# Performance work log

Measured on AMD Instinct MI355X. Metric: run time of the kernel, lower is better.

The kernel has to match this reference:

```python
import jax, jax.numpy as jnp
import numpy as np

S = 32            # state: nodes per graph, conv output channels
B = 4096          # number of graphs
N = B * S         # total nodes
E = 2 * 1024 * 1024  # total edges (avg degree 16)
A = 2             # action_space_dimension
NACT = 32         # number_of_actions (adv heads)
EPS = 1e-5


def setup_inputs() -> dict:
    key = jax.random.key(0)
    ks = jax.random.split(key, 24)
    f = lambda k, sh, s: (jax.random.normal(k, sh, jnp.float32) * s)
    return {
        'x': f(ks[0], (N, 2), 1.0),
        'edge_index': jax.random.randint(ks[1], (2, E), 0, N),
        # conv1 MLP: Linear(4,16) -> ReLU -> Linear(16,S)
        'c1W1': f(ks[2], (4, 16), 0.5), 'c1b1': jnp.zeros((16,), jnp.float32),
        'c1W2': f(ks[3], (16, S), 0.25), 'c1b2': jnp.zeros((S,), jnp.float32),
        # conv2/conv3 MLPs: Linear(2*S,16) -> ReLU -> Linear(16,S)
        'c2W1': f(ks[4], (2 * S, 16), 0.12), 'c2b1': jnp.zeros((16,), jnp.float32),
        'c2W2': f(ks[5], (16, S), 0.25), 'c2b2': jnp.zeros((S,), jnp.float32),
        'c3W1': f(ks[6], (2 * S, 16), 0.12), 'c3b1': jnp.zeros((16,), jnp.float32),
        'c3W2': f(ks[7], (16, S), 0.25), 'c3b2': jnp.zeros((S,), jnp.float32),
        # 3 BatchNorm1d(S) layers (stacked)
        'bn_g': jnp.ones((3, S), jnp.float32), 'bn_b': jnp.zeros((3, S), jnp.float32),
        # dense head MLP 1024->256->256->256
        'mW1': f(ks[8], (S * S, 256), 0.03), 'mb1': jnp.zeros((256,), jnp.float32),
        'mW2': f(ks[9], (256, 256), 0.06), 'mb2': jnp.zeros((256,), jnp.float32),
        'mW3': f(ks[10], (256, 256), 0.06), 'mb3': jnp.zeros((256,), jnp.float32),
        # dueling heads
        'vW': f(ks[11], (256, 1), 0.06), 'vb': jnp.zeros((1,), jnp.float32),
        'aW': f(ks[12], (NACT, 256, A), 0.06), 'ab': jnp.zeros((NACT, A), jnp.float32),
    }


def _edgeconv(x, src, dst, W1, b1, W2, b2):
    # PyG EdgeConv with aggr='add': msg = MLP(cat[x_i, x_j - x_i]), summed at target i
    xi = x[dst]                       # [E, F]
    xj = x[src]                       # [E, F]
    m = jnp.concatenate([xi, xj - xi], axis=-1)        # [E, 2F]
    h = jnp.maximum(m @ W1 + b1, 0.0) @ W2 + b2        # [E, S]
    return jax.ops.segment_sum(h, dst, num_segments=x.shape[0])  # [N, S]


def _bn(h, g, b):
    # BatchNorm1d in training mode: batch stats over node dim, biased variance
    mu = h.mean(axis=0)
    var = jnp.mean((h - mu) ** 2, axis=0)
    return (h - mu) * jax.lax.rsqrt(var + EPS) * g + b


def reference(x, edge_index, c1W1, c1b1, c1W2, c1b2, c2W1, c2b1, c2W2, c2b2,
              c3W1, c3b1, c3W2, c3b2, bn_g, bn_b, mW1, mb1, mW2, mb2,
              mW3, mb3, vW, vb, aW, ab):
    src, dst = edge_index[0], edge_index[1]
    h = _edgeconv(x, src, dst, c1W1, c1b1, c1W2, c1b2)
    h = jax.nn.relu(_bn(h, bn_g[0], bn_b[0]))
    h = _edgeconv(h, src, dst, c2W1, c2b1, c2W2, c2b2)
    h = jax.nn.relu(_bn(h, bn_g[1], bn_b[1]))
    h = _edgeconv(h, src, dst, c3W1, c3b1, c3W2, c3b2)
    h = jax.nn.relu(_bn(h, bn_g[2], bn_b[2]))
    nb = x.shape[0] // S                                 # graphs in batch
    out = h.reshape(nb, S * S)                           # [B, in_size]
    out = jax.nn.relu(out @ mW1 + mb1)
    out = jax.nn.relu(out @ mW2 + mb2)
    out = jax.nn.relu(out @ mW3 + mb3)                   # [B, 256]
    value = out @ vW + vb                                # [B, 1]
    adv = jnp.einsum('bf,nfa->bna', out, aW) + ab        # [B, NACT, A]
    q = value[:, :, None] + adv - adv.mean(axis=2, keepdims=True)
    return q
```

## Files before the change

### kernel.cpp

```cpp
#include <hip/hip_runtime.h>
#include <hip/hip_fp16.h>

#define NN 131072
#define EE 2097152
#define SS 32
#define HH 16
#define BB 4096
#define EPS 1e-5f

#define BKT 512
#define BNODES 256
#define CAP 4864
#define SCAP 8192
#define TILE 8192

typedef _Float16 f16x8 __attribute__((ext_vector_type(8)));
typedef _Float16 f16x4 __attribute__((ext_vector_type(4)));
typedef float f32x4 __attribute__((ext_vector_type(4)));

__global__ __launch_bounds__(1024) void k_bsort(const int* __restrict__ ei, int* __restrict__ gcount,
                                                int* __restrict__ words) {
    __shared__ int cnt[BKT];
    __shared__ int tstart[BKT];
    __shared__ int gshift[BKT];
    __shared__ int sc[BKT];
    __shared__ int sword[TILE];
    __shared__ int sdst[TILE];
    int t = threadIdx.x;
    if (t < BKT) cnt[t] = 0;
    __syncthreads();
    int e0 = blockIdx.x * TILE;
    int dreg[TILE / 1024];
#pragma unroll
    for (int it = 0; it < TILE / 1024; ++it) {
        dreg[it] = ei[EE + e0 + it * 1024 + t];
        atomicAdd(&cnt[dreg[it] >> 8], 1);
    }
    __syncthreads();
    int val = (t < BKT) ? cnt[t] : 0;
    if (t < BKT) sc[t] = val;
    __syncthreads();
    for (int d = 1; d < BKT; d <<= 1) {
        int v2 = (t >= d && t < BKT) ? sc[t - d] : 0;
        __syncthreads();
        if (t < BKT) sc[t] += v2;
        __syncthreads();
    }
    if (t < BKT) {
        int excl = sc[t] - val;
        tstart[t] = excl;
        gshift[t] = t * CAP + atomicAdd(&gcount[t], val) - excl;
        cnt[t] = 0;
    }
    __syncthreads();
#pragma unroll
    for (int it = 0; it < TILE / 1024; ++it) {
        int e = e0 + it * 1024 + t;
        int src = ei[e];
        int dst = dreg[it];
        int b = dst >> 8;
        int r = atomicAdd(&cnt[b], 1);
        int p = tstart[b] + r;
        sword[p] = src | ((dst & 255) << 17);
        sdst[p] = gshift[b] + p;
    }
    __syncthreads();
#pragma unroll
    for (int it = 0; it < TILE / 1024; ++it) {
        int i = it * 1024 + t;
        words[sdst[i]] = sword[i];
    }
}

__global__ __launch_bounds__(512) void k_csr(const int* __restrict__ words, const int* __restrict__ gcount,
                                             int* __restrict__ ssrc, int* __restrict__ offs,
                                             int* __restrict__ offe) {
    __shared__ int hist[BNODES];
    __shared__ int sc[BNODES];
    __shared__ int base[BNODES];
    int t = threadIdx.x;
    int b = blockIdx.x;
    if (t < BNODES) hist[t] = 0;
    __syncthreads();
    int cnt = gcount[b];
    const int* wp = words + (size_t)b * CAP;
    int wreg[10];
#pragma unroll
    for (int it = 0; it < 10; ++it) {
        int p = t + it * 512;
        int w = (p < cnt) ? wp[p] : -1;
        wreg[it] = w;
        if (w >= 0) atomicAdd(&hist[w >> 17], 1);
    }
    __syncthreads();
    int val = 0, pval = 0;
    if (t < BNODES) {
        val = hist[t];
        pval = (val + 15) & ~15;
        sc[t] = pval;
    }
    __syncthreads();
    for (int d = 1; d < BNODES; d <<= 1) {
        int v2 = (t >= d && t < BNODES) ? sc[t - d] : 0;
        __syncthreads();
        if (t < BNODES) sc[t] += v2;
        __syncthreads();
    }
    int gbase = b * SCAP;
    if (t < BNODES) {
        base[t] = sc[t] - pval;
        offs[b * BNODES + t] = gbase + base[t];
        offe[b * BNODES + t] = gbase + base[t] + val;
        hist[t] = 0;
    }
    __syncthreads();
#pragma unroll
    for (int it = 0; it < 10; ++it) {
        int w = wreg[it];
        if (w >= 0) {
            int dl = w >> 17;
            int r = atomicAdd(&hist[dl], 1);
            ssrc[gbase + base[dl] + r] = w & 0x1FFFF;
        }
    }
    if (t < BNODES) {
        int s = gbase + base[t];
        for (int i = val; i < pval; ++i) ssrc[s + i] = NN;
    }
}

__global__ __launch_bounds__(256) void k_prep(const float* __restrict__ mW1, const float* __restrict__ mW2,
                                              const float* __restrict__ mW3, const float* __restrict__ vW,
                                              const float* __restrict__ vb, const float* __restrict__ aW,
                                              const float* __restrict__ ab,
                                              _Float16* __restrict__ W1T, _Float16* __restrict__ W2T,
                                              _Float16* __restrict__ W3T, _Float16* __restrict__ BqT,
                                              float* __restrict__ biasq, int* __restrict__ gcount,
                                              float* __restrict__ bns,
                                              const float* __restrict__ x, const float* __restrict__ c1W1,
                                              const float* __restrict__ c1b1,
                                              float* __restrict__ u, __half* __restrict__ v) {
    int i = blockIdx.x * 256 + threadIdx.x;
    {
        int n = i >> 4, c = i & 15;
        float x0 = x[n * 2], x1 = x[n * 2 + 1];
        float w0 = c1W1[c], w1 = c1W1[16 + c], w2 = c1W1[32 + c], w3 = c1W1[48 + c];
        u[i] = c1b1[c] + x0 * (w0 - w2) + x1 * (w1 - w3);
        v[i] = __float2half(x0 * w2 + x1 * w3);
    }
    if (i < 262144) {
        int k = i >> 8, n = i & 255;
        W1T[(size_t)n * 1024 + k] = (_Float16)mW1[i];
    }
    if (i < 65536) {
        int k = i >> 8, n = i & 255;
        W2T[n * 256 + k] = (_Float16)mW2[i];
        W3T[n * 256 + k] = (_Float16)mW3[i];
    }
    if (i < 16384) {
        int f = i >> 6, j = i & 63;
        int n = j >> 1, a = j & 1;
        float wa = aW[n * 512 + f * 2 + a];
        float wo = aW[n * 512 + f * 2 + (1 - a)];
        BqT[j * 256 + f] = (_Float16)(vW[f] + 0.5f * (wa - wo));
    }
    if (i < 64) biasq[i] = vb[0] + 0.5f * (ab[i] - ab[i ^ 1]);
    if (i < 512) gcount[i] = 0;
    if (i < 1536) bns[i] = 0.f;
    if (i < 16) v[NN * 16 + i] = __float2half(-60000.0f);
}

__global__ __launch_bounds__(256) void k_bnpre(const float* __restrict__ y, const float* __restrict__ bns,
                                               const float* __restrict__ g, const float* __restrict__ bb,
                                               const float* __restrict__ W1, const float* __restrict__ b1,
                                               float* __restrict__ u, __half* __restrict__ v) {
    __shared__ float sh[16][33];
    __shared__ float wd[32][16];
    __shared__ float wv[32][16];
    __shared__ float scL[32], soL[32];
    int t = threadIdx.x;
    if (t < 32) {
        float sm = 0.f, sq = 0.f;
#pragma unroll
        for (int s = 0; s < 8; ++s) { sm += bns[s * 64 + t]; sq += bns[s * 64 + 32 + t]; }
        const float inv_n = 1.0f / (float)NN;
        float mean = sm * inv_n;
        float var = sq * inv_n - mean * mean;
        float s2 = g[t] * rsqrtf(var + EPS);
        scL[t] = s2;
        soL[t] = bb[t] - mean * s2;
    }
    for (int i = t; i < 512; i += 256) {
        int f = i >> 4, c = i & 15;
        float wt = W1[i];
        float wb = W1[512 + i];
        wd[f][c] = wt - wb;
        wv[f][c] = wb;
    }
    __syncthreads();
    int nb = blockIdx.x * 16;
    for (int i = t; i < 512; i += 256) {
        int col = i & 31;
        sh[i >> 5][col] = fmaxf(y[nb * 32 + i] * scL[col] + soL[col], 0.f);
    }
    __syncthreads();
    int c = t & 15, nl = t >> 4;
    float uu = b1[c], vv = 0.f;
#pragma unroll
    for (int f = 0; f < 32; ++f) {
        float hv = sh[nl][f];
        uu += hv * wd[f][c];
        vv += hv * wv[f][c];
    }
    int n = nb + nl;
    u[n * 16 + c] = uu;
    v[n * 16 + c] = __float2half(vv);
    if (blockIdx.x == 0 && t < 16) v[NN * 16 + t] = __float2half(-60000.0f);
}

__global__ __launch_bounds__(256) void k_gather(const float* __restrict__ u, const __half* __restrict__ v,
                                                const int* __restrict__ ssrc, const int* __restrict__ offs,
                                                const int* __restrict__ offe,
                                                const float* __restrict__ W2, const float* __restrict__ b2,
                                                float* __restrict__ y, float* __restrict__ bns) {
    __shared__ float sw2[512];
    __shared__ float sagg[32 * 18];
    __shared__ float cntL[32];
    __shared__ float ssum[32];
    __shared__ float ssq[32];
    int t = threadIdx.x;
    if (t < 32) { ssum[t] = 0.f; ssq[t] = 0.f; }
    float w2a = W2[t], w2b = W2[t + 256];
    float b2r0 = b2[(t & 7) * 4], b2r1 = b2[(t & 7) * 4 + 1];
    float b2r2 = b2[(t & 7) * 4 + 2], b2r3 = b2[(t & 7) * 4 + 3];
    int nl = t >> 3, c2 = t & 7;
    int n = blockIdx.x * 32 + nl;
    int s0 = offs[n], e0 = offe[n];
    int pe = s0 + ((e0 - s0 + 15) & ~15);
    float2 uc = *(const float2*)(u + (size_t)n * 16 + 2 * c2);
    float a0 = 0.f, a1 = 0.f;
    for (int p = s0; p < pe; p += 16) {
        int idx[16];
#pragma unroll
        for (int i = 0; i < 16; ++i) idx[i] = ssrc[p + i];
        float2 vv[16];
#pragma unroll
        for (int i = 0; i < 16; ++i)
            vv[i] = __half22float2(*(const __half2*)(v + (size_t)idx[i] * 16 + 2 * c2));
#pragma unroll
        for (int i = 0; i < 16; ++i) {
            a0 += fmaxf(uc.x + vv[i].x, 0.f);
            a1 += fmaxf(uc.y + vv[i].y, 0.f);
        }
    }
    sagg[nl * 18 + 2 * c2] = a0;
    sagg[nl * 18 + 2 * c2 + 1] = a1;
    if (c2 == 0) cntL[nl] = (float)(e0 - s0);
    sw2[t] = w2a;
    sw2[t + 256] = w2b;
    __syncthreads();
    int node = t >> 3, oc = (t & 7) * 4;
    float cw = cntL[node];
    float o0 = b2r0 * cw, o1 = b2r1 * cw, o2 = b2r2 * cw, o3 = b2r3 * cw;
#pragma unroll
    for (int k = 0; k < 16; ++k) {
        float a = sagg[node * 18 + k];
        o0 += a * sw2[k * 32 + oc];
        o1 += a * sw2[k * 32 + oc + 1];
        o2 += a * sw2[k * 32 + oc + 2];
        o3 += a * sw2[k * 32 + oc + 3];
    }
    *(float4*)(y + (size_t)(blockIdx.x * 32 + node) * 32 + oc) = make_float4(o0, o1, o2, o3);
    float q0 = o0 * o0, q1 = o1 * o1, q2 = o2 * o2, q3 = o3 * o3;
#pragma unroll
    for (int m = 8; m < 64; m <<= 1) {
        o0 += __shfl_xor(o0, m); o1 += __shfl_xor(o1, m);
        o2 += __shfl_xor(o2, m); o3 += __shfl_xor(o3, m);
        q0 += __shfl_xor(q0, m); q1 += __shfl_xor(q1, m);
        q2 += __shfl_xor(q2, m); q3 += __shfl_xor(q3, m);
    }
    if ((t & 63) < 8) {
        atomicAdd(&ssum[oc], o0);     atomicAdd(&ssum[oc + 1], o1);
        atomicAdd(&ssum[oc + 2], o2); atomicAdd(&ssum[oc + 3], o3);
        atomicAdd(&ssq[oc], q0);      atomicAdd(&ssq[oc + 1], q1);
        atomicAdd(&ssq[oc + 2], q2);  atomicAdd(&ssq[oc + 3], q3);
    }
    __syncthreads();
    if (t < 64) {
        float val = (t < 32) ? ssum[t] : ssq[t - 32];
        atomicAdd(&bns[(blockIdx.x & 7) * 64 + t], val);
    }
}

__global__ __launch_bounds__(256) void k_bnrelu16(const float* __restrict__ y, const float* __restrict__ bns,
                                                  const float* __restrict__ g, const float* __restrict__ bb,
                                                  _Float16* __restrict__ h16) {
    __shared__ float sc_[32], sh_[32];
    int t = threadIdx.x;
    if (t < 32) {
        float sm = 0.f, sq = 0.f;
#pragma unroll
        for (int s = 0; s < 8; ++s) { sm += bns[s * 64 + t]; sq += bns[s * 64 + 32 + t]; }
        const float inv_n = 1.0f / (float)NN;
        float mean = sm * inv_n;
        float var = sq * inv_n - mean * mean;
        float sc = g[t] * rsqrtf(var + EPS);
        sc_[t] = sc;
        sh_[t] = bb[t] - mean * sc;
    }
    __syncthreads();
    int i = (blockIdx.x * 256 + t) * 4;
    float4 v4 = *(const float4*)(y + i);
    int j = i & 31;
    f16x4 o;
    o[0] = (_Float16)fmaxf(v4.x * sc_[j] + sh_[j], 0.f);
    o[1] = (_Float16)fmaxf(v4.y * sc_[j + 1] + sh_[j + 1], 0.f);
    o[2] = (_Float16)fmaxf(v4.z * sc_[j + 2] + sh_[j + 2], 0.f);
    o[3] = (_Float16)fmaxf(v4.w * sc_[j + 3] + sh_[j + 3], 0.f);
    *(f16x4*)(h16 + i) = o;
}

__global__ __launch_bounds__(256) void k_mgemm(const _Float16* __restrict__ A, const _Float16* __restrict__ BT,
                                               const float* __restrict__ bias, float* __restrict__ Cf,
                                               _Float16* __restrict__ Ch, int M, int N, int K,
                                               int relu, int out16) {
    int tid = threadIdx.x;
    int w = tid >> 6, l = tid & 63, q = l >> 4, r = l & 15;
    int rowBase = blockIdx.x * 64;
    int col = blockIdx.y * 64 + w * 16 + r;
    const _Float16* ap = A + (size_t)(rowBase + r) * K + q * 8;
    const _Float16* bp = BT + (size_t)col * K + q * 8;
    f32x4 z = {0.f, 0.f, 0.f, 0.f};
    f32x4 acc[4] = {z, z, z, z};
    for (int k0 = 0; k0 < K; k0 += 32) {
        f16x8 bf = *(const f16x8*)(bp + k0);
        f16x8 a0 = *(const f16x8*)(ap + k0);
        f16x8 a1 = *(const f16x8*)(ap + k0 + (size_t)16 * K);
        f16x8 a2 = *(const f16x8*)(ap + k0 + (size_t)32 * K);
        f16x8 a3 = *(const f16x8*)(ap + k0 + (size_t)48 * K);
        acc[0] = __builtin_amdgcn_mfma_f32_16x16x32_f16(a0, bf, acc[0], 0, 0, 0);
        acc[1] = __builtin_amdgcn_mfma_f32_16x16x32_f16(a1, bf, acc[1], 0, 0, 0);
        acc[2] = __builtin_amdgcn_mfma_f32_16x16x32_f16(a2, bf, acc[2], 0, 0, 0);
        acc[3] = __builtin_amdgcn_mfma_f32_16x16x32_f16(a3, bf, acc[3], 0, 0, 0);
    }
    float bv = bias[col];
#pragma unroll
    for (int rt = 0; rt < 4; ++rt) {
#pragma unroll
        for (int i = 0; i < 4; ++i) {
            int row = rowBase + rt * 16 + q * 4 + i;
            float val = acc[rt][i] + bv;
            if (relu) val = fmaxf(val, 0.f);
            if (out16) Ch[(size_t)row * N + col] = (_Float16)val;
            else       Cf[(size_t)row * N + col] = val;
        }
    }
}

extern "C" void kernel_launch(void* const* d_in, const int* in_sizes, int n_in,
                              void* d_out, int out_size, void* d_ws, size_t ws_size,
                              hipStream_t stream) {
    const float* x    = (const float*)d_in[0];
    const int*   ei   = (const int*)d_in[1];
    const float* c1W1 = (const float*)d_in[2];
    const float* c1b1 = (const float*)d_in[3];
    const float* c1W2 = (const float*)d_in[4];
    const float* c1b2 = (const float*)d_in[5];
    const float* c2W1 = (const float*)d_in[6];
    const float* c2b1 = (const float*)d_in[7];
    const float* c2W2 = (const float*)d_in[8];
    const float* c2b2 = (const float*)d_in[9];
    const float* c3W1 = (const float*)d_in[10];
    const float* c3b1 = (const float*)d_in[11];
    const float* c3W2 = (const float*)d_in[12];
    const float* c3b2 = (const float*)d_in[13];
    const float* bn_g = (const float*)d_in[14];
    const float* bn_b = (const float*)d_in[15];
    const float* mW1  = (const float*)d_in[16];
    const float* mb1  = (const float*)d_in[17];
    const float* mW2  = (const float*)d_in[18];
    const float* mb2  = (const float*)d_in[19];
    const float* mW3  = (const float*)d_in[20];
    const float* mb3  = (const float*)d_in[21];
    const float* vW   = (const float*)d_in[22];
    const float* vb   = (const float*)d_in[23];
    const float* aW   = (const float*)d_in[24];
    const float* ab   = (const float*)d_in[25];
    float* out = (float*)d_out;

    char* p = (char*)d_ws;
    auto take = [&](size_t bytes) {
        char* r = p;
        p += (bytes + 255) & ~(size_t)255;
        return r;
    };
    int*       gcount = (int*)take((size_t)BKT * 4);
    int*       words  = (int*)take((size_t)BKT * CAP * 4);
    int*       ssrc   = (int*)take((size_t)BKT * SCAP * 4);
    int*       offs   = (int*)take((size_t)NN * 4);
    int*       offe   = (int*)take((size_t)NN * 4);
    float*     u      = (float*)take((size_t)NN * HH * 4);
    __half*    v      = (__half*)take((size_t)(NN + 1) * HH * 2);
    float*     y      = (float*)take((size_t)NN * SS * 4);
    _Float16*  h16    = (_Float16*)take((size_t)NN * SS * 2);
    float*     bns    = (float*)take(3 * 512 * 4);
    _Float16*  W1T    = (_Float16*)take((size_t)256 * 1024 * 2);
    _Float16*  W2T    = (_Float16*)take((size_t)256 * 256 * 2);
    _Float16*  W3T    = (_Float16*)take((size_t)256 * 256 * 2);
    _Float16*  BqT    = (_Float16*)take((size_t)64 * 256 * 2);
    float*     biasq  = (float*)take(64 * 4);
    _Float16*  Xa     = (_Float16*)take((size_t)BB * 256 * 2);
    _Float16*  Xb     = (_Float16*)take((size_t)BB * 256 * 2);

    k_prep<<<NN * 16 / 256, 256, 0, stream>>>(mW1, mW2, mW3, vW, vb, aW, ab,
                                              W1T, W2T, W3T, BqT, biasq, gcount, bns,
                                              x, c1W1, c1b1, u, v);

    k_bsort<<<EE / TILE, 1024, 0, stream>>>(ei, gcount, words);
    k_csr<<<BKT, 512, 0, stream>>>(words, gcount, ssrc, offs, offe);

    k_gather<<<NN / 32, 256, 0, stream>>>(u, v, ssrc, offs, offe, c1W2, c1b2, y, bns);
    k_bnpre<<<NN / 16, 256, 0, stream>>>(y, bns, bn_g, bn_b, c2W1, c2b1, u, v);
    k_gather<<<NN / 32, 256, 0, stream>>>(u, v, ssrc, offs, offe, c2W2, c2b2, y, bns + 512);
    k_bnpre<<<NN / 16, 256, 0, stream>>>(y, bns + 512, bn_g + 32, bn_b + 32, c3W1, c3b1, u, v);
    k_gather<<<NN / 32, 256, 0, stream>>>(u, v, ssrc, offs, offe, c3W2, c3b2, y, bns + 1024);
    k_bnrelu16<<<NN * 32 / 1024, 256, 0, stream>>>(y, bns + 1024, bn_g + 64, bn_b + 64, h16);

    k_mgemm<<<dim3(BB / 64, 4), 256, 0, stream>>>(h16, W1T, mb1, nullptr, Xa, BB, 256, 1024, 1, 1);
    k_mgemm<<<dim3(BB / 64, 4), 256, 0, stream>>>(Xa, W2T, mb2, nullptr, Xb, BB, 256, 256, 1, 1);
    k_mgemm<<<dim3(BB / 64, 4), 256, 0, stream>>>(Xb, W3T, mb3, nullptr, Xa, BB, 256, 256, 1, 1);
    k_mgemm<<<dim3(BB / 64, 1), 256, 0, stream>>>(Xa, BqT, biasq, out, nullptr, BB, 64, 256, 0, 0);
}
```

Baseline: 307.0 us.

## Fuse dense MLP head into one kernel and widen gather loads per thread

The four separate MFMA GEMM launches for the dense head become one kernel in which each block keeps a 32-row tile of activations in shared memory across all layers, so the intermediate activation buffers never go to global memory and three launches are dropped. The gather kernel now gives each thread four channels of a node, 64 nodes per block, and loads 8-byte fp16 vectors instead of 4-byte ones, which halves the number of scattered loads per edge. In exchange the fused MLP launches only 128 blocks, which limits parallelism, and each block re-reads the full weight matrices.

```diff
diff --git a/kernel.cpp b/kernel.cpp
--- a/kernel.cpp
+++ b/kernel.cpp
@@ -224,8 +224,8 @@
                                                 const float* __restrict__ W2, const float* __restrict__ b2,
                                                 float* __restrict__ y, float* __restrict__ bns) {
     __shared__ float sw2[512];
-    __shared__ float sagg[32 * 18];
-    __shared__ float cntL[32];
+    __shared__ float sagg[64 * 17];
+    __shared__ float cntL[64];
     __shared__ float ssum[32];
     __shared__ float ssq[32];
     int t = threadIdx.x;
@@ -233,57 +233,66 @@
     float w2a = W2[t], w2b = W2[t + 256];
     float b2r0 = b2[(t & 7) * 4], b2r1 = b2[(t & 7) * 4 + 1];
     float b2r2 = b2[(t & 7) * 4 + 2], b2r3 = b2[(t & 7) * 4 + 3];
-    int nl = t >> 3, c2 = t & 7;
-    int n = blockIdx.x * 32 + nl;
+    int nl = t >> 2, c4 = t & 3;
+    int n = blockIdx.x * 64 + nl;
     int s0 = offs[n], e0 = offe[n];
     int pe = s0 + ((e0 - s0 + 15) & ~15);
-    float2 uc = *(const float2*)(u + (size_t)n * 16 + 2 * c2);
-    float a0 = 0.f, a1 = 0.f;
+    float4 uc = *(const float4*)(u + (size_t)n * 16 + 4 * c4);
+    float a0 = 0.f, a1 = 0.f, a2 = 0.f, a3 = 0.f;
     for (int p = s0; p < pe; p += 16) {
         int idx[16];
 #pragma unroll
         for (int i = 0; i < 16; ++i) idx[i] = ssrc[p + i];
-        float2 vv[16];
+        uint2 hv[16];
 #pragma unroll
         for (int i = 0; i < 16; ++i)
-            vv[i] = __half22float2(*(const __half2*)(v + (size_t)idx[i] * 16 + 2 * c2));
+            hv[i] = *(const uint2*)(v + (size_t)idx[i] * 16 + 4 * c4);
 #pragma unroll
         for (int i = 0; i < 16; ++i) {
-            a0 += fmaxf(uc.x + vv[i].x, 0.f);
-            a1 += fmaxf(uc.y + vv[i].y, 0.f);
-        }
-    }
-    sagg[nl * 18 + 2 * c2] = a0;
-    sagg[nl * 18 + 2 * c2 + 1] = a1;
-    if (c2 == 0) cntL[nl] = (float)(e0 - s0);
+            float2 f01 = __half22float2(*(const __half2*)&hv[i].x);
+            float2 f23 = __half22float2(*(const __half2*)&hv[i].y);
+            a0 += fmaxf(uc.x + f01.x, 0.f);
+            a1 += fmaxf(uc.y + f01.y, 0.f);
+            a2 += fmaxf(uc.z + f23.x, 0.f);
+            a3 += fmaxf(uc.w + f23.y, 0.f);
+        }
+    }
+    sagg[nl * 17 + 4 * c4]     = a0;
+    sagg[nl * 17 + 4 * c4 + 1] = a1;
+    sagg[nl * 17 + 4 * c4 + 2] = a2;
+    sagg[nl * 17 + 4 * c4 + 3] = a3;
+    if (c4 == 0) cntL[nl] = (float)(e0 - s0);
     sw2[t] = w2a;
     sw2[t + 256] = w2b;
     __syncthreads();
-    int node = t >> 3, oc = (t & 7) * 4;
-    float cw = cntL[node];
-    float o0 = b2r0 * cw, o1 = b2r1 * cw, o2 = b2r2 * cw, o3 = b2r3 * cw;
-#pragma unroll
-    for (int k = 0; k < 16; ++k) {
-        float a = sagg[node * 18 + k];
-        o0 += a * sw2[k * 32 + oc];
-        o1 += a * sw2[k * 32 + oc + 1];
-        o2 += a * sw2[k * 32 + oc + 2];
-        o3 += a * sw2[k * 32 + oc + 3];
-    }
-    *(float4*)(y + (size_t)(blockIdx.x * 32 + node) * 32 + oc) = make_float4(o0, o1, o2, o3);
-    float q0 = o0 * o0, q1 = o1 * o1, q2 = o2 * o2, q3 = o3 * o3;
-#pragma unroll
-    for (int m = 8; m < 64; m <<= 1) {
-        o0 += __shfl_xor(o0, m); o1 += __shfl_xor(o1, m);
-        o2 += __shfl_xor(o2, m); o3 += __shfl_xor(o3, m);
-        q0 += __shfl_xor(q0, m); q1 += __shfl_xor(q1, m);
-        q2 += __shfl_xor(q2, m); q3 += __shfl_xor(q3, m);
-    }
-    if ((t & 63) < 8) {
-        atomicAdd(&ssum[oc], o0);     atomicAdd(&ssum[oc + 1], o1);
-        atomicAdd(&ssum[oc + 2], o2); atomicAdd(&ssum[oc + 3], o3);
-        atomicAdd(&ssq[oc], q0);      atomicAdd(&ssq[oc + 1], q1);
-        atomicAdd(&ssq[oc + 2], q2);  atomicAdd(&ssq[oc + 3], q3);
+#pragma unroll
+    for (int h = 0; h < 2; ++h) {
+        int node = h * 32 + (t >> 3), oc = (t & 7) * 4;
+        float cw = cntL[node];
+        float o0 = b2r0 * cw, o1 = b2r1 * cw, o2 = b2r2 * cw, o3 = b2r3 * cw;
+#pragma unroll
+        for (int k = 0; k < 16; ++k) {
+            float a = sagg[node * 17 + k];
+            o0 += a * sw2[k * 32 + oc];
+            o1 += a * sw2[k * 32 + oc + 1];
+            o2 += a * sw2[k * 32 + oc + 2];
+            o3 += a * sw2[k * 32 + oc + 3];
+        }
+        *(float4*)(y + (size_t)(blockIdx.x * 64 + node) * 32 + oc) = make_float4(o0, o1, o2, o3);
+        float q0 = o0 * o0, q1 = o1 * o1, q2 = o2 * o2, q3 = o3 * o3;
+#pragma unroll
+        for (int m = 8; m < 64; m <<= 1) {
+            o0 += __shfl_xor(o0, m); o1 += __shfl_xor(o1, m);
+            o2 += __shfl_xor(o2, m); o3 += __shfl_xor(o3, m);
+            q0 += __shfl_xor(q0, m); q1 += __shfl_xor(q1, m);
+            q2 += __shfl_xor(q2, m); q3 += __shfl_xor(q3, m);
+        }
+        if ((t & 63) < 8) {
+            atomicAdd(&ssum[oc], o0);     atomicAdd(&ssum[oc + 1], o1);
+            atomicAdd(&ssum[oc + 2], o2); atomicAdd(&ssum[oc + 3], o3);
+            atomicAdd(&ssq[oc], q0);      atomicAdd(&ssq[oc + 1], q1);
+            atomicAdd(&ssq[oc + 2], q2);  atomicAdd(&ssq[oc + 3], q3);
+        }
     }
     __syncthreads();
     if (t < 64) {
@@ -320,40 +329,116 @@
     *(f16x4*)(h16 + i) = o;
 }
 
-__global__ __launch_bounds__(256) void k_mgemm(const _Float16* __restrict__ A, const _Float16* __restrict__ BT,
-                                               const float* __restrict__ bias, float* __restrict__ Cf,
-                                               _Float16* __restrict__ Ch, int M, int N, int K,
-                                               int relu, int out16) {
+__global__ __launch_bounds__(256) void k_mlp(const _Float16* __restrict__ A, const _Float16* __restrict__ W1T,
+                                             const _Float16* __restrict__ W2T, const _Float16* __restrict__ W3T,
+                                             const _Float16* __restrict__ BqT,
+                                             const float* __restrict__ mb1, const float* __restrict__ mb2,
+                                             const float* __restrict__ mb3, const float* __restrict__ biasq,
+                                             float* __restrict__ out) {
+    __shared__ _Float16 sX[32 * 264];
+    __shared__ _Float16 sY[32 * 264];
     int tid = threadIdx.x;
     int w = tid >> 6, l = tid & 63, q = l >> 4, r = l & 15;
-    int rowBase = blockIdx.x * 64;
-    int col = blockIdx.y * 64 + w * 16 + r;
-    const _Float16* ap = A + (size_t)(rowBase + r) * K + q * 8;
-    const _Float16* bp = BT + (size_t)col * K + q * 8;
+    int rowBase = blockIdx.x * 32;
     f32x4 z = {0.f, 0.f, 0.f, 0.f};
-    f32x4 acc[4] = {z, z, z, z};
-    for (int k0 = 0; k0 < K; k0 += 32) {
-        f16x8 bf = *(const f16x8*)(bp + k0);
-        f16x8 a0 = *(const f16x8*)(ap + k0);
-        f16x8 a1 = *(const f16x8*)(ap + k0 + (size_t)16 * K);
-        f16x8 a2 = *(const f16x8*)(ap + k0 + (size_t)32 * K);
-        f16x8 a3 = *(const f16x8*)(ap + k0 + (size_t)48 * K);
-        acc[0] = __builtin_amdgcn_mfma_f32_16x16x32_f16(a0, bf, acc[0], 0, 0, 0);
-        acc[1] = __builtin_amdgcn_mfma_f32_16x16x32_f16(a1, bf, acc[1], 0, 0, 0);
-        acc[2] = __builtin_amdgcn_mfma_f32_16x16x32_f16(a2, bf, acc[2], 0, 0, 0);
-        acc[3] = __builtin_amdgcn_mfma_f32_16x16x32_f16(a3, bf, acc[3], 0, 0, 0);
-    }
-    float bv = bias[col];
-#pragma unroll
-    for (int rt = 0; rt < 4; ++rt) {
-#pragma unroll
-        for (int i = 0; i < 4; ++i) {
-            int row = rowBase + rt * 16 + q * 4 + i;
-            float val = acc[rt][i] + bv;
-            if (relu) val = fmaxf(val, 0.f);
-            if (out16) Ch[(size_t)row * N + col] = (_Float16)val;
-            else       Cf[(size_t)row * N + col] = val;
-        }
+
+    {
+        f32x4 acc[2][4] = {{z, z, z, z}, {z, z, z, z}};
+        const _Float16* ap = A + (size_t)(rowBase + r) * 1024 + q * 8;
+        for (int k0 = 0; k0 < 1024; k0 += 32) {
+            f16x8 a0 = *(const f16x8*)(ap + k0);
+            f16x8 a1 = *(const f16x8*)(ap + k0 + (size_t)16 * 1024);
+#pragma unroll
+            for (int ct = 0; ct < 4; ++ct) {
+                int col = ct * 64 + w * 16 + r;
+                f16x8 bf = *(const f16x8*)(W1T + (size_t)col * 1024 + q * 8 + k0);
+                acc[0][ct] = __builtin_amdgcn_mfma_f32_16x16x32_f16(a0, bf, acc[0][ct], 0, 0, 0);
+                acc[1][ct] = __builtin_amdgcn_mfma_f32_16x16x32_f16(a1, bf, acc[1][ct], 0, 0, 0);
+            }
+        }
+#pragma unroll
+        for (int ct = 0; ct < 4; ++ct) {
+            int col = ct * 64 + w * 16 + r;
+            float bv = mb1[col];
+#pragma unroll
+            for (int rt = 0; rt < 2; ++rt)
+#pragma unroll
+                for (int i = 0; i < 4; ++i)
+                    sX[(rt * 16 + q * 4 + i) * 264 + col] = (_Float16)fmaxf(acc[rt][ct][i] + bv, 0.f);
+        }
+    }
+    __syncthreads();
+
+    {
+        f32x4 acc[2][4] = {{z, z, z, z}, {z, z, z, z}};
+        for (int k0 = 0; k0 < 256; k0 += 32) {
+            f16x8 a0 = *(const f16x8*)(sX + r * 264 + q * 8 + k0);
+            f16x8 a1 = *(const f16x8*)(sX + (16 + r) * 264 + q * 8 + k0);
+#pragma unroll
+            for (int ct = 0; ct < 4; ++ct) {
+                int col = ct * 64 + w * 16 + r;
+                f16x8 bf = *(const f16x8*)(W2T + (size_t)col * 256 + q * 8 + k0);
+                acc[0][ct] = __builtin_amdgcn_mfma_f32_16x16x32_f16(a0, bf, acc[0][ct], 0, 0, 0);
+                acc[1][ct] = __builtin_amdgcn_mfma_f32_16x16x32_f16(a1, bf, acc[1][ct], 0, 0, 0);
+            }
+        }
+        __syncthreads();
+#pragma unroll
+        for (int ct = 0; ct < 4; ++ct) {
+            int col = ct * 64 + w * 16 + r;
+            float bv = mb2[col];
+#pragma unroll
+            for (int rt = 0; rt < 2; ++rt)
+#pragma unroll
+                for (int i = 0; i < 4; ++i)
+                    sY[(rt * 16 + q * 4 + i) * 264 + col] = (_Float16)fmaxf(acc[rt][ct][i] + bv, 0.f);
+        }
+    }
+    __syncthreads();
+
+    {
+        f32x4 acc[2][4] = {{z, z, z, z}, {z, z, z, z}};
+        for (int k0 = 0; k0 < 256; k0 += 32) {
+            f16x8 a0 = *(const f16x8*)(sY + r * 264 + q * 8 + k0);
+            f16x8 a1 = *(const f16x8*)(sY + (16 + r) * 264 + q * 8 + k0);
+#pragma unroll
+            for (int ct = 0; ct < 4; ++ct) {
+                int col = ct * 64 + w * 16 + r;
+                f16x8 bf = *(const f16x8*)(W3T + (size_t)col * 256 + q * 8 + k0);
+                acc[0][ct] = __builtin_amdgcn_mfma_f32_16x16x32_f16(a0, bf, acc[0][ct], 0, 0, 0);
+                acc[1][ct] = __builtin_amdgcn_mfma_f32_16x16x32_f16(a1, bf, acc[1][ct], 0, 0, 0);
+            }
+        }
+        __syncthreads();
+#pragma unroll
+        for (int ct = 0; ct < 4; ++ct) {
+            int col = ct * 64 + w * 16 + r;
+            float bv = mb3[col];
+#pragma unroll
+            for (int rt = 0; rt < 2; ++rt)
+#pragma unroll
+                for (int i = 0; i < 4; ++i)
+                    sX[(rt * 16 + q * 4 + i) * 264 + col] = (_Float16)fmaxf(acc[rt][ct][i] + bv, 0.f);
+        }
+    }
+    __syncthreads();
+
+    {
+        f32x4 acc[2] = {z, z};
+        int col = w * 16 + r;
+        for (int k0 = 0; k0 < 256; k0 += 32) {
+            f16x8 a0 = *(const f16x8*)(sX + r * 264 + q * 8 + k0);
+            f16x8 a1 = *(const f16x8*)(sX + (16 + r) * 264 + q * 8 + k0);
+            f16x8 bf = *(const f16x8*)(BqT + (size_t)col * 256 + q * 8 + k0);
+            acc[0] = __builtin_amdgcn_mfma_f32_16x16x32_f16(a0, bf, acc[0], 0, 0, 0);
+            acc[1] = __builtin_amdgcn_mfma_f32_16x16x32_f16(a1, bf, acc[1], 0, 0, 0);
+        }
+        float bv = biasq[col];
+#pragma unroll
+        for (int rt = 0; rt < 2; ++rt)
+#pragma unroll
+            for (int i = 0; i < 4; ++i)
+                out[(size_t)(rowBase + rt * 16 + q * 4 + i) * 64 + col] = acc[rt][i] + bv;
     }
 }
 
@@ -409,8 +494,6 @@
     _Float16*  W3T    = (_Float16*)take((size_t)256 * 256 * 2);
     _Float16*  BqT    = (_Float16*)take((size_t)64 * 256 * 2);
     float*     biasq  = (float*)take(64 * 4);
-    _Float16*  Xa     = (_Float16*)take((size_t)BB * 256 * 2);
-    _Float16*  Xb     = (_Float16*)take((size_t)BB * 256 * 2);
 
     k_prep<<<NN * 16 / 256, 256, 0, stream>>>(mW1, mW2, mW3, vW, vb, aW, ab,
                                               W1T, W2T, W3T, BqT, biasq, gcount, bns,
@@ -419,15 +502,12 @@
     k_bsort<<<EE / TILE, 1024, 0, stream>>>(ei, gcount, words);
     k_csr<<<BKT, 512, 0, stream>>>(words, gcount, ssrc, offs, offe);
 
-    k_gather<<<NN / 32, 256, 0, stream>>>(u, v, ssrc, offs, offe, c1W2, c1b2, y, bns);
+    k_gather<<<NN / 64, 256, 0, stream>>>(u, v, ssrc, offs, offe, c1W2, c1b2, y, bns);
     k_bnpre<<<NN / 16, 256, 0, stream>>>(y, bns, bn_g, bn_b, c2W1, c2b1, u, v);
-    k_gather<<<NN / 32, 256, 0, stream>>>(u, v, ssrc, offs, offe, c2W2, c2b2, y, bns + 512);
+    k_gather<<<NN / 64, 256, 0, stream>>>(u, v, ssrc, offs, offe, c2W2, c2b2, y, bns + 512);
     k_bnpre<<<NN / 16, 256, 0, stream>>>(y, bns + 512, bn_g + 32, bn_b + 32, c3W1, c3b1, u, v);
-    k_gather<<<NN / 32, 256, 0, stream>>>(u, v, ssrc, offs, offe, c3W2, c3b2, y, bns + 1024);
+    k_gather<<<NN / 64, 256, 0, stream>>>(u, v, ssrc, offs, offe, c3W2, c3b2, y, bns + 1024);
     k_bnrelu16<<<NN * 32 / 1024, 256, 0, stream>>>(y, bns + 1024, bn_g + 64, bn_b + 64, h16);
 
-    k_mgemm<<<dim3(BB / 64, 4), 256, 0, stream>>>(h16, W1T, mb1, nullptr, Xa, BB, 256, 1024, 1, 1);
-    k_mgemm<<<dim3(BB / 64, 4), 256, 0, stream>>>(Xa, W2T, mb2, nullptr, Xb, BB, 256, 256, 1, 1);
-    k_mgemm<<<dim3(BB / 64, 4), 256, 0, stream>>>(Xb, W3T, mb3, nullptr, Xa, BB, 256, 256, 1, 1);
-    k_mgemm<<<dim3(BB / 64, 1), 256, 0, stream>>>(Xa, BqT, biasq, out, nullptr, BB, 64, 256, 0, 0);
-}
+    k_mlp<<<BB / 32, 256, 0, stream>>>(h16, W1T, W2T, W3T, BqT, mb1, mb2, mb3, biasq, out);
+}
```

Result: no change. 307.6 us (+0.2%).
